# Optimization experiments

Hardware: AMD Instinct MI355X
Metric: run time of the kernel (lower is better)

Reference implementation:

```python
import jax, jax.numpy as jnp
import numpy as np

B, N, C = 1, 50000, 128
E, D = 800000, 2


def setup_inputs() -> dict:
    key = jax.random.key(0)
    k1, k2, k3 = jax.random.split(key, 3)
    x = jax.random.normal(k1, (B, N, C), dtype=jnp.float32)
    edge_weights = jax.random.normal(k2, (B, E, D), dtype=jnp.float32)
    directed_edges = jax.random.randint(k3, (B, E, 2), 0, N, dtype=jnp.int64)
    return {"x": x, "edge_weights": edge_weights, "directed_edges": directed_edges}


def reference(x, edge_weights, directed_edges):
    # x: [B, N, C] node features; edge_weights: [B, E, D]; directed_edges: [B, E, 2] = (target, source)
    b, n, c = x.shape
    _, e, d = edge_weights.shape
    target = directed_edges[..., 0]  # [B, E]
    source = directed_edges[..., 1]  # [B, E]
    bidx = jnp.arange(b)[:, None]  # [B, 1] broadcasts against [B, E]
    # gather node diffs per edge: [B, E, C]
    diff = x[bidx, source] - x[bidx, target]
    # weight by edge direction vector and flatten (C, D) -> C*D, matching torch reshape order
    message = jnp.einsum('bed,bec->becd', edge_weights, diff).reshape(b, e, c * d)
    # scatter-add into per-node gradient accumulator: [B, N, C*D]
    out = jnp.zeros((b, n, c * d), dtype=message.dtype)
    out = out.at[bidx, target].add(message)
    return out
```

## Files before the change

### kernel.cpp

```cpp
#include <hip/hip_runtime.h>


#define CAP 64
#define SCAN_TILE 512

__device__ __forceinline__ void gather_accum(const float* __restrict__ x,
                                             const int4* __restrict__ rec,
                                             int beg, int end, int lane,
                                             float& a0, float& a1, float& a2,
                                             float& a3, float& swx, float& swy) {
  int i = beg;
  for (; i + 4 <= end; i += 4) {
    const int4 r0 = rec[i];
    const int4 r1 = rec[i + 1];
    const int4 r2 = rec[i + 2];
    const int4 r3 = rec[i + 3];
    const float2 x0 = *reinterpret_cast<const float2*>(x + (size_t)r0.x * 128 + 2 * lane);
    const float2 x1 = *reinterpret_cast<const float2*>(x + (size_t)r1.x * 128 + 2 * lane);
    const float2 x2 = *reinterpret_cast<const float2*>(x + (size_t)r2.x * 128 + 2 * lane);
    const float2 x3 = *reinterpret_cast<const float2*>(x + (size_t)r3.x * 128 + 2 * lane);
    const float w0x = __int_as_float(r0.y), w0y = __int_as_float(r0.z);
    const float w1x = __int_as_float(r1.y), w1y = __int_as_float(r1.z);
    const float w2x = __int_as_float(r2.y), w2y = __int_as_float(r2.z);
    const float w3x = __int_as_float(r3.y), w3y = __int_as_float(r3.z);
    a0 += w0x * x0.x; a1 += w0y * x0.x; a2 += w0x * x0.y; a3 += w0y * x0.y;
    swx += w0x; swy += w0y;
    a0 += w1x * x1.x; a1 += w1y * x1.x; a2 += w1x * x1.y; a3 += w1y * x1.y;
    swx += w1x; swy += w1y;
    a0 += w2x * x2.x; a1 += w2y * x2.x; a2 += w2x * x2.y; a3 += w2y * x2.y;
    swx += w2x; swy += w2y;
    a0 += w3x * x3.x; a1 += w3y * x3.x; a2 += w3x * x3.y; a3 += w3y * x3.y;
    swx += w3x; swy += w3y;
  }
  for (; i < end; ++i) {
    const int4 r0 = rec[i];
    const float2 x0 = *reinterpret_cast<const float2*>(x + (size_t)r0.x * 128 + 2 * lane);
    const float w0x = __int_as_float(r0.y), w0y = __int_as_float(r0.z);
    a0 += w0x * x0.x; a1 += w0y * x0.x; a2 += w0x * x0.y; a3 += w0y * x0.y;
    swx += w0x; swy += w0y;
  }
}

__device__ __forceinline__ void gather_store(const float* __restrict__ x,
                                             float* __restrict__ out, int node,
                                             int lane, float a0, float a1, float a2,
                                             float a3, float swx, float swy) {
  const float2 xt = *reinterpret_cast<const float2*>(x + (size_t)node * 128 + 2 * lane);
  float4 o;
  o.x = a0 - swx * xt.x;
  o.y = a1 - swy * xt.x;
  o.z = a2 - swx * xt.y;
  o.w = a3 - swy * xt.y;
  *reinterpret_cast<float4*>(out + (size_t)node * 256 + 4 * lane) = o;
}

__global__ __launch_bounds__(256) void k_append(const int* __restrict__ edges,
                                                const float2* __restrict__ ew,
                                                int* __restrict__ counts,
                                                int4* __restrict__ rec, int E) {
  int e = blockIdx.x * blockDim.x + threadIdx.x;
  if (e >= E) return;
  const int2 ts = *reinterpret_cast<const int2*>(edges + 2ll * e);
  const float2 w = ew[e];
  const int pos = atomicAdd(&counts[ts.x], 1);
  if (pos < CAP) {
    int4 r;
    r.x = ts.y;
    r.y = __float_as_int(w.x);
    r.z = __float_as_int(w.y);
    r.w = 0;
    rec[(size_t)ts.x * CAP + pos] = r;
  }
}

__global__ __launch_bounds__(256) void k_gather_b(const float* __restrict__ x,
                                                  const int* __restrict__ counts,
                                                  const int4* __restrict__ rec,
                                                  float* __restrict__ out, int n) {
  const int lane = threadIdx.x & 63;
  const int node = (blockIdx.x * blockDim.x + threadIdx.x) >> 6;
  if (node >= n) return;
  const int deg = min(counts[node], CAP);
  const int beg = node * CAP;
  float a0 = 0.f, a1 = 0.f, a2 = 0.f, a3 = 0.f, swx = 0.f, swy = 0.f;
  gather_accum(x, rec, beg, beg + deg, lane, a0, a1, a2, a3, swx, swy);
  gather_store(x, out, node, lane, a0, a1, a2, a3, swx, swy);
}

__global__ __launch_bounds__(256) void k_hist(const int* __restrict__ edges,
                                              int* __restrict__ counts, int E) {
  int i = blockIdx.x * blockDim.x + threadIdx.x;
  int e = 2 * i;
  if (e + 1 < E) {
    int4 p = *reinterpret_cast<const int4*>(edges + 2ll * e);
    atomicAdd(&counts[p.x], 1);
    atomicAdd(&counts[p.z], 1);
  } else if (e < E) {
    atomicAdd(&counts[edges[2ll * e]], 1);
  }
}

__global__ __launch_bounds__(256) void k_part(const int* __restrict__ counts,
                                              int* __restrict__ partials, int n) {
  __shared__ int red[256];
  const int t = threadIdx.x;
  const int base = blockIdx.x * SCAN_TILE;
  int v = 0;
  int i0 = base + t, i1 = base + 256 + t;
  if (i0 < n) v += counts[i0];
  if (i1 < n) v += counts[i1];
  red[t] = v;
  __syncthreads();
  for (int s = 128; s > 0; s >>= 1) {
    if (t < s) red[t] += red[t + s];
    __syncthreads();
  }
  if (t == 0) partials[blockIdx.x] = red[0];
}

__global__ __launch_bounds__(1024) void k_scanp(int* __restrict__ partials, int P) {
  __shared__ int tile[1024];
  const int t = threadIdx.x;
  int v = (t < P) ? partials[t] : 0;
  tile[t] = v;
  __syncthreads();
  for (int off = 1; off < 1024; off <<= 1) {
    int u = (t >= off) ? tile[t - off] : 0;
    __syncthreads();
    tile[t] += u;
    __syncthreads();
  }
  if (t < P) partials[t] = tile[t] - v;
}

__global__ __launch_bounds__(256) void k_apply(const int* __restrict__ counts,
                                               const int* __restrict__ partials,
                                               int* __restrict__ offs,
                                               int* __restrict__ cursor, int n, int E) {
  __shared__ int tile[256];
  const int t = threadIdx.x;
  const int base = blockIdx.x * SCAN_TILE;
  const int ia = base + 2 * t, ib = ia + 1;
  int a = (ia < n) ? counts[ia] : 0;
  int b = (ib < n) ? counts[ib] : 0;
  int s = a + b;
  tile[t] = s;
  __syncthreads();
  for (int off = 1; off < 256; off <<= 1) {
    int u = (t >= off) ? tile[t - off] : 0;
    __syncthreads();
    tile[t] += u;
    __syncthreads();
  }
  const int excl = tile[t] - s;
  const int o = partials[blockIdx.x] + excl;
  if (ia < n) { offs[ia] = o; cursor[ia] = o; }
  if (ib < n) { offs[ib] = o + a; cursor[ib] = o + a; }
  if (blockIdx.x == 0 && t == 0) offs[n] = E;
}

__global__ __launch_bounds__(256) void k_scatter(const int* __restrict__ edges,
                                                 const float2* __restrict__ ew,
                                                 int* __restrict__ cursor,
                                                 int4* __restrict__ rec, int E) {
  int e = blockIdx.x * blockDim.x + threadIdx.x;
  if (e >= E) return;
  int2 ts = *reinterpret_cast<const int2*>(edges + 2ll * e);
  float2 w = ew[e];
  int pos = atomicAdd(&cursor[ts.x], 1);
  int4 r;
  r.x = ts.y;
  r.y = __float_as_int(w.x);
  r.z = __float_as_int(w.y);
  r.w = 0;
  rec[pos] = r;
}

__global__ __launch_bounds__(256) void k_gather_s(const float* __restrict__ x,
                                                  const int* __restrict__ offs,
                                                  const int4* __restrict__ rec,
                                                  float* __restrict__ out, int n) {
  const int lane = threadIdx.x & 63;
  const int node = (blockIdx.x * blockDim.x + threadIdx.x) >> 6;
  if (node >= n) return;
  float a0 = 0.f, a1 = 0.f, a2 = 0.f, a3 = 0.f, swx = 0.f, swy = 0.f;
  gather_accum(x, rec, offs[node], offs[node + 1], lane, a0, a1, a2, a3, swx, swy);
  gather_store(x, out, node, lane, a0, a1, a2, a3, swx, swy);
}

__global__ __launch_bounds__(256) void k_atomic(const float* __restrict__ x,
                                                const float* __restrict__ ew,
                                                const int* __restrict__ edges,
                                                float* __restrict__ out, int E) {
  const int lane = threadIdx.x & 63;
  const int wave = (blockIdx.x * blockDim.x + threadIdx.x) >> 6;
  const int nwaves = (gridDim.x * blockDim.x) >> 6;
  for (int e = wave; e < E; e += nwaves) {
    const int2 ts = *reinterpret_cast<const int2*>(edges + 2ll * e);
    const float2 w = *reinterpret_cast<const float2*>(ew + 2ll * e);
    const float2 vs = *reinterpret_cast<const float2*>(x + (size_t)ts.y * 128 + 2 * lane);
    const float2 vt = *reinterpret_cast<const float2*>(x + (size_t)ts.x * 128 + 2 * lane);
    const float d0 = vs.x - vt.x;
    const float d1 = vs.y - vt.y;
    float* o = out + (size_t)ts.x * 256 + 4 * lane;
    unsafeAtomicAdd(o + 0, w.x * d0);
    unsafeAtomicAdd(o + 1, w.y * d0);
    unsafeAtomicAdd(o + 2, w.x * d1);
    unsafeAtomicAdd(o + 3, w.y * d1);
  }
}

extern "C" void kernel_launch(void* const* d_in, const int* in_sizes, int n_in,
                              void* d_out, int out_size, void* d_ws, size_t ws_size,
                              hipStream_t stream) {
  const float* x = (const float*)d_in[0];
  const float* ewf = (const float*)d_in[1];
  const int* edges = (const int*)d_in[2];
  float* out = (float*)d_out;
  const float2* ew = (const float2*)ewf;

  const int E = in_sizes[1] / 2;
  const int N = in_sizes[0] / 128;

  size_t cnt_sec = ((size_t)N * 4 + 15) & ~(size_t)15;
  size_t need_bucket = cnt_sec + (size_t)N * CAP * 16;

  if (ws_size >= need_bucket) {
    char* wsb = (char*)d_ws;
    int* counts = (int*)wsb;
    int4* rec = (int4*)(wsb + cnt_sec);
    hipMemsetAsync(counts, 0, (size_t)N * 4, stream);
    k_append<<<(E + 255) / 256, 256, 0, stream>>>(edges, ew, counts, rec, E);
    k_gather_b<<<(N * 64 + 255) / 256, 256, 0, stream>>>(x, counts, rec, out, N);
    return;
  }

  const int P = (N + SCAN_TILE - 1) / SCAN_TILE;
  size_t int_sec = ((size_t)(3 * N + 1 + P) * 4 + 15) & ~(size_t)15;
  size_t need_sort = int_sec + (size_t)E * 16;

  if (ws_size >= need_sort) {
    char* wsb = (char*)d_ws;
    int* counts = (int*)wsb;
    int* offs = counts + N;
    int* cursor = offs + N + 1;
    int* partials = cursor + N;
    int4* rec = (int4*)(wsb + int_sec);
    hipMemsetAsync(counts, 0, (size_t)N * 4, stream);
    k_hist<<<((E + 1) / 2 + 255) / 256, 256, 0, stream>>>(edges, counts, E);
    k_part<<<P, 256, 0, stream>>>(counts, partials, N);
    k_scanp<<<1, 1024, 0, stream>>>(partials, P);
    k_apply<<<P, 256, 0, stream>>>(counts, partials, offs, cursor, N, E);
    k_scatter<<<(E + 255) / 256, 256, 0, stream>>>(edges, ew, cursor, rec, E);
    k_gather_s<<<(N * 64 + 255) / 256, 256, 0, stream>>>(x, offs, rec, out, N);
    return;
  }

  hipMemsetAsync(d_out, 0, (size_t)out_size * sizeof(float), stream);
  k_atomic<<<2048, 256, 0, stream>>>(x, ewf, edges, out, E);
}
```

Before: 115.3 us.

## Bucket edge indices instead of full records and split wave over two edges

The bucket path now stores only a 4-byte edge index per slot instead of a 16-byte record, so the append kernel writes far less and handles two edges per thread. The gather kernel loads one bucket entry per lane, looks up the source and weights, broadcasts them with shuffles, and has each half-wave process a different edge with float4 loads. A cross-half shuffle reduction then combines the partial sums before the store. In exchange, the gather does an extra indirect read of edges and weights, and the unrolled gather_accum used by the sort fallback path is simplified to a plain loop.

New measurement: 150.4 us. 30.5% more time.

```diff
diff --git a/kernel.cpp b/kernel.cpp
--- a/kernel.cpp
+++ b/kernel.cpp
@@ -3,88 +3,121 @@
 
 #define CAP 64
 #define SCAN_TILE 512
+
+__global__ __launch_bounds__(256) void k_append2(const int* __restrict__ edges,
+                                                 int* __restrict__ counts,
+                                                 int* __restrict__ idxb, int E) {
+  const int i = blockIdx.x * blockDim.x + threadIdx.x;
+  const int e = 2 * i;
+  if (e + 1 < E) {
+    const int4 p = *reinterpret_cast<const int4*>(edges + 2ll * e);
+    const int p0 = atomicAdd(&counts[p.x], 1);
+    if (p0 < CAP) idxb[p.x * CAP + p0] = e;
+    const int p1 = atomicAdd(&counts[p.z], 1);
+    if (p1 < CAP) idxb[p.z * CAP + p1] = e + 1;
+  } else if (e < E) {
+    const int t = edges[2ll * e];
+    const int p0 = atomicAdd(&counts[t], 1);
+    if (p0 < CAP) idxb[t * CAP + p0] = e;
+  }
+}
+
+#define ACC(xr, wx, wy)                                              \
+  a0 += (wx) * (xr).x; a1 += (wy) * (xr).x;                          \
+  a2 += (wx) * (xr).y; a3 += (wy) * (xr).y;                          \
+  a4 += (wx) * (xr).z; a5 += (wy) * (xr).z;                          \
+  a6 += (wx) * (xr).w; a7 += (wy) * (xr).w;                          \
+  swx += (wx); swy += (wy);
+
+__global__ __launch_bounds__(256) void k_gather2(const float* __restrict__ x,
+                                                 const int* __restrict__ counts,
+                                                 const int* __restrict__ idxb,
+                                                 const int* __restrict__ edges,
+                                                 const float2* __restrict__ ew,
+                                                 float* __restrict__ out, int n) {
+  const int lane = threadIdx.x & 63;
+  const int node = (blockIdx.x * blockDim.x + threadIdx.x) >> 6;
+  if (node >= n) return;
+  const int c = lane & 31;
+  const int half = lane >> 5;
+
+  const int deg = min(counts[node], CAP);
+
+  float a0 = 0.f, a1 = 0.f, a2 = 0.f, a3 = 0.f;
+  float a4 = 0.f, a5 = 0.f, a6 = 0.f, a7 = 0.f;
+  float swx = 0.f, swy = 0.f;
+
+  if (deg > 0) {
+    const int li = min(lane, deg - 1);
+    const int e = idxb[node * CAP + li];
+    const int srcl = edges[2 * e + 1];
+    const float2 wl = ew[e];
+
+    const int nfull = deg >> 1;
+    int i = 0;
+    for (; i + 2 <= nfull; i += 2) {
+      const int m0 = 2 * i + half;
+      const int m1 = m0 + 2;
+      const int s0 = __shfl(srcl, m0);
+      const float w0x = __shfl(wl.x, m0);
+      const float w0y = __shfl(wl.y, m0);
+      const int s1 = __shfl(srcl, m1);
+      const float w1x = __shfl(wl.x, m1);
+      const float w1y = __shfl(wl.y, m1);
+      const float4 x0 = *reinterpret_cast<const float4*>(x + (size_t)s0 * 128 + 4 * c);
+      const float4 x1 = *reinterpret_cast<const float4*>(x + (size_t)s1 * 128 + 4 * c);
+      ACC(x0, w0x, w0y)
+      ACC(x1, w1x, w1y)
+    }
+    if (i < nfull) {
+      const int m0 = 2 * i + half;
+      const int s0 = __shfl(srcl, m0);
+      const float w0x = __shfl(wl.x, m0);
+      const float w0y = __shfl(wl.y, m0);
+      const float4 x0 = *reinterpret_cast<const float4*>(x + (size_t)s0 * 128 + 4 * c);
+      ACC(x0, w0x, w0y)
+    }
+    if (deg & 1) {
+      const int m = deg - 1;
+      const int s0 = __shfl(srcl, m);
+      float w0x = __shfl(wl.x, m);
+      float w0y = __shfl(wl.y, m);
+      if (half) { w0x = 0.f; w0y = 0.f; }
+      const float4 x0 = *reinterpret_cast<const float4*>(x + (size_t)s0 * 128 + 4 * c);
+      ACC(x0, w0x, w0y)
+    }
+  }
+
+  a0 += __shfl_xor(a0, 32); a1 += __shfl_xor(a1, 32);
+  a2 += __shfl_xor(a2, 32); a3 += __shfl_xor(a3, 32);
+  a4 += __shfl_xor(a4, 32); a5 += __shfl_xor(a5, 32);
+  a6 += __shfl_xor(a6, 32); a7 += __shfl_xor(a7, 32);
+  swx += __shfl_xor(swx, 32); swy += __shfl_xor(swy, 32);
+
+  const float4 xt = *reinterpret_cast<const float4*>(x + (size_t)node * 128 + 4 * c);
+  float4 o;
+  if (half == 0) {
+    o.x = a0 - swx * xt.x; o.y = a1 - swy * xt.x;
+    o.z = a2 - swx * xt.y; o.w = a3 - swy * xt.y;
+  } else {
+    o.x = a4 - swx * xt.z; o.y = a5 - swy * xt.z;
+    o.z = a6 - swx * xt.w; o.w = a7 - swy * xt.w;
+  }
+  *reinterpret_cast<float4*>(out + (size_t)node * 256 + 8 * c + 4 * half) = o;
+}
 
 __device__ __forceinline__ void gather_accum(const float* __restrict__ x,
                                              const int4* __restrict__ rec,
                                              int beg, int end, int lane,
                                              float& a0, float& a1, float& a2,
                                              float& a3, float& swx, float& swy) {
-  int i = beg;
-  for (; i + 4 <= end; i += 4) {
-    const int4 r0 = rec[i];
-    const int4 r1 = rec[i + 1];
-    const int4 r2 = rec[i + 2];
-    const int4 r3 = rec[i + 3];
-    const float2 x0 = *reinterpret_cast<const float2*>(x + (size_t)r0.x * 128 + 2 * lane);
-    const float2 x1 = *reinterpret_cast<const float2*>(x + (size_t)r1.x * 128 + 2 * lane);
-    const float2 x2 = *reinterpret_cast<const float2*>(x + (size_t)r2.x * 128 + 2 * lane);
-    const float2 x3 = *reinterpret_cast<const float2*>(x + (size_t)r3.x * 128 + 2 * lane);
-    const float w0x = __int_as_float(r0.y), w0y = __int_as_float(r0.z);
-    const float w1x = __int_as_float(r1.y), w1y = __int_as_float(r1.z);
-    const float w2x = __int_as_float(r2.y), w2y = __int_as_float(r2.z);
-    const float w3x = __int_as_float(r3.y), w3y = __int_as_float(r3.z);
-    a0 += w0x * x0.x; a1 += w0y * x0.x; a2 += w0x * x0.y; a3 += w0y * x0.y;
-    swx += w0x; swy += w0y;
-    a0 += w1x * x1.x; a1 += w1y * x1.x; a2 += w1x * x1.y; a3 += w1y * x1.y;
-    swx += w1x; swy += w1y;
-    a0 += w2x * x2.x; a1 += w2y * x2.x; a2 += w2x * x2.y; a3 += w2y * x2.y;
-    swx += w2x; swy += w2y;
-    a0 += w3x * x3.x; a1 += w3y * x3.x; a2 += w3x * x3.y; a3 += w3y * x3.y;
-    swx += w3x; swy += w3y;
-  }
-  for (; i < end; ++i) {
+  for (int i = beg; i < end; ++i) {
     const int4 r0 = rec[i];
     const float2 x0 = *reinterpret_cast<const float2*>(x + (size_t)r0.x * 128 + 2 * lane);
     const float w0x = __int_as_float(r0.y), w0y = __int_as_float(r0.z);
     a0 += w0x * x0.x; a1 += w0y * x0.x; a2 += w0x * x0.y; a3 += w0y * x0.y;
     swx += w0x; swy += w0y;
   }
-}
-
-__device__ __forceinline__ void gather_store(const float* __restrict__ x,
-                                             float* __restrict__ out, int node,
-                                             int lane, float a0, float a1, float a2,
-                                             float a3, float swx, float swy) {
-  const float2 xt = *reinterpret_cast<const float2*>(x + (size_t)node * 128 + 2 * lane);
-  float4 o;
-  o.x = a0 - swx * xt.x;
-  o.y = a1 - swy * xt.x;
-  o.z = a2 - swx * xt.y;
-  o.w = a3 - swy * xt.y;
-  *reinterpret_cast<float4*>(out + (size_t)node * 256 + 4 * lane) = o;
-}
-
-__global__ __launch_bounds__(256) void k_append(const int* __restrict__ edges,
-                                                const float2* __restrict__ ew,
-                                                int* __restrict__ counts,
-                                                int4* __restrict__ rec, int E) {
-  int e = blockIdx.x * blockDim.x + threadIdx.x;
-  if (e >= E) return;
-  const int2 ts = *reinterpret_cast<const int2*>(edges + 2ll * e);
-  const float2 w = ew[e];
-  const int pos = atomicAdd(&counts[ts.x], 1);
-  if (pos < CAP) {
-    int4 r;
-    r.x = ts.y;
-    r.y = __float_as_int(w.x);
-    r.z = __float_as_int(w.y);
-    r.w = 0;
-    rec[(size_t)ts.x * CAP + pos] = r;
-  }
-}
-
-__global__ __launch_bounds__(256) void k_gather_b(const float* __restrict__ x,
-                                                  const int* __restrict__ counts,
-                                                  const int4* __restrict__ rec,
-                                                  float* __restrict__ out, int n) {
-  const int lane = threadIdx.x & 63;
-  const int node = (blockIdx.x * blockDim.x + threadIdx.x) >> 6;
-  if (node >= n) return;
-  const int deg = min(counts[node], CAP);
-  const int beg = node * CAP;
-  float a0 = 0.f, a1 = 0.f, a2 = 0.f, a3 = 0.f, swx = 0.f, swy = 0.f;
-  gather_accum(x, rec, beg, beg + deg, lane, a0, a1, a2, a3, swx, swy);
-  gather_store(x, out, node, lane, a0, a1, a2, a3, swx, swy);
 }
 
 __global__ __launch_bounds__(256) void k_hist(const int* __restrict__ edges,
@@ -185,7 +218,13 @@
   if (node >= n) return;
   float a0 = 0.f, a1 = 0.f, a2 = 0.f, a3 = 0.f, swx = 0.f, swy = 0.f;
   gather_accum(x, rec, offs[node], offs[node + 1], lane, a0, a1, a2, a3, swx, swy);
-  gather_store(x, out, node, lane, a0, a1, a2, a3, swx, swy);
+  const float2 xt = *reinterpret_cast<const float2*>(x + (size_t)node * 128 + 2 * lane);
+  float4 o;
+  o.x = a0 - swx * xt.x;
+  o.y = a1 - swy * xt.x;
+  o.z = a2 - swx * xt.y;
+  o.w = a3 - swy * xt.y;
+  *reinterpret_cast<float4*>(out + (size_t)node * 256 + 4 * lane) = o;
 }
 
 __global__ __launch_bounds__(256) void k_atomic(const float* __restrict__ x,
@@ -223,15 +262,15 @@
   const int N = in_sizes[0] / 128;
 
   size_t cnt_sec = ((size_t)N * 4 + 15) & ~(size_t)15;
-  size_t need_bucket = cnt_sec + (size_t)N * CAP * 16;
+  size_t need_bucket = cnt_sec + (size_t)N * CAP * 4;
 
   if (ws_size >= need_bucket) {
     char* wsb = (char*)d_ws;
     int* counts = (int*)wsb;
-    int4* rec = (int4*)(wsb + cnt_sec);
+    int* idxb = (int*)(wsb + cnt_sec);
     hipMemsetAsync(counts, 0, (size_t)N * 4, stream);
-    k_append<<<(E + 255) / 256, 256, 0, stream>>>(edges, ew, counts, rec, E);
-    k_gather_b<<<(N * 64 + 255) / 256, 256, 0, stream>>>(x, counts, rec, out, N);
+    k_append2<<<((E + 1) / 2 + 255) / 256, 256, 0, stream>>>(edges, counts, idxb, E);
+    k_gather2<<<(N * 64 + 255) / 256, 256, 0, stream>>>(x, counts, idxb, edges, ew, out, N);
     return;
   }
 
```

## Stage bucket records in LDS and split wave into half-waves over float4 rows

Applied to the files above, without the earlier changes.

The bucketed gather kernel now loads each node's edge records once per wave, one per lane, into shared memory. The weight sums come from a wave shuffle reduction instead of per-lane serial accumulation. Each half-wave handles alternating edges with float4 row loads and eight accumulators, and the two halves are combined with a shuffle at the end. This replaces redundant broadcast reads of the record list from global memory and halves the per-edge loop trip count, at the cost of a block-level barrier, more registers and extra shuffles. The sorted-path gather is inlined and loses its 4-way unrolling.

Result: no change. 113.4 us (-1.6%).

```diff
diff --git a/kernel.cpp b/kernel.cpp
--- a/kernel.cpp
+++ b/kernel.cpp
@@ -3,64 +3,14 @@
 
 #define CAP 64
 #define SCAN_TILE 512
-
-__device__ __forceinline__ void gather_accum(const float* __restrict__ x,
-                                             const int4* __restrict__ rec,
-                                             int beg, int end, int lane,
-                                             float& a0, float& a1, float& a2,
-                                             float& a3, float& swx, float& swy) {
-  int i = beg;
-  for (; i + 4 <= end; i += 4) {
-    const int4 r0 = rec[i];
-    const int4 r1 = rec[i + 1];
-    const int4 r2 = rec[i + 2];
-    const int4 r3 = rec[i + 3];
-    const float2 x0 = *reinterpret_cast<const float2*>(x + (size_t)r0.x * 128 + 2 * lane);
-    const float2 x1 = *reinterpret_cast<const float2*>(x + (size_t)r1.x * 128 + 2 * lane);
-    const float2 x2 = *reinterpret_cast<const float2*>(x + (size_t)r2.x * 128 + 2 * lane);
-    const float2 x3 = *reinterpret_cast<const float2*>(x + (size_t)r3.x * 128 + 2 * lane);
-    const float w0x = __int_as_float(r0.y), w0y = __int_as_float(r0.z);
-    const float w1x = __int_as_float(r1.y), w1y = __int_as_float(r1.z);
-    const float w2x = __int_as_float(r2.y), w2y = __int_as_float(r2.z);
-    const float w3x = __int_as_float(r3.y), w3y = __int_as_float(r3.z);
-    a0 += w0x * x0.x; a1 += w0y * x0.x; a2 += w0x * x0.y; a3 += w0y * x0.y;
-    swx += w0x; swy += w0y;
-    a0 += w1x * x1.x; a1 += w1y * x1.x; a2 += w1x * x1.y; a3 += w1y * x1.y;
-    swx += w1x; swy += w1y;
-    a0 += w2x * x2.x; a1 += w2y * x2.x; a2 += w2x * x2.y; a3 += w2y * x2.y;
-    swx += w2x; swy += w2y;
-    a0 += w3x * x3.x; a1 += w3y * x3.x; a2 += w3x * x3.y; a3 += w3y * x3.y;
-    swx += w3x; swy += w3y;
-  }
-  for (; i < end; ++i) {
-    const int4 r0 = rec[i];
-    const float2 x0 = *reinterpret_cast<const float2*>(x + (size_t)r0.x * 128 + 2 * lane);
-    const float w0x = __int_as_float(r0.y), w0y = __int_as_float(r0.z);
-    a0 += w0x * x0.x; a1 += w0y * x0.x; a2 += w0x * x0.y; a3 += w0y * x0.y;
-    swx += w0x; swy += w0y;
-  }
-}
-
-__device__ __forceinline__ void gather_store(const float* __restrict__ x,
-                                             float* __restrict__ out, int node,
-                                             int lane, float a0, float a1, float a2,
-                                             float a3, float swx, float swy) {
-  const float2 xt = *reinterpret_cast<const float2*>(x + (size_t)node * 128 + 2 * lane);
-  float4 o;
-  o.x = a0 - swx * xt.x;
-  o.y = a1 - swy * xt.x;
-  o.z = a2 - swx * xt.y;
-  o.w = a3 - swy * xt.y;
-  *reinterpret_cast<float4*>(out + (size_t)node * 256 + 4 * lane) = o;
-}
 
 __global__ __launch_bounds__(256) void k_append(const int* __restrict__ edges,
                                                 const float2* __restrict__ ew,
                                                 int* __restrict__ counts,
                                                 int4* __restrict__ rec, int E) {
-  int e = blockIdx.x * blockDim.x + threadIdx.x;
+  const int e = blockIdx.x * blockDim.x + threadIdx.x;
   if (e >= E) return;
-  const int2 ts = *reinterpret_cast<const int2*>(edges + 2ll * e);
+  const int2 ts = reinterpret_cast<const int2*>(edges)[e];
   const float2 w = ew[e];
   const int pos = atomicAdd(&counts[ts.x], 1);
   if (pos < CAP) {
@@ -73,18 +23,93 @@
   }
 }
 
-__global__ __launch_bounds__(256) void k_gather_b(const float* __restrict__ x,
-                                                  const int* __restrict__ counts,
-                                                  const int4* __restrict__ rec,
-                                                  float* __restrict__ out, int n) {
+#define ACC8(X, WX, WY)                                  \
+  a0 = fmaf((WX), (X).x, a0); a1 = fmaf((WY), (X).x, a1); \
+  a2 = fmaf((WX), (X).y, a2); a3 = fmaf((WY), (X).y, a3); \
+  a4 = fmaf((WX), (X).z, a4); a5 = fmaf((WY), (X).z, a5); \
+  a6 = fmaf((WX), (X).w, a6); a7 = fmaf((WY), (X).w, a7);
+
+__device__ __forceinline__ float4 ldrow(const float* __restrict__ x, int src, int c) {
+  return *reinterpret_cast<const float4*>(x + (size_t)src * 128 + 4 * c);
+}
+
+__global__ __launch_bounds__(256) void k_gather3(const float* __restrict__ x,
+                                                 const int* __restrict__ counts,
+                                                 const int4* __restrict__ rec,
+                                                 float* __restrict__ out, int n) {
+  __shared__ int4 smem[4][CAP];
   const int lane = threadIdx.x & 63;
+  const int wid = threadIdx.x >> 6;
   const int node = (blockIdx.x * blockDim.x + threadIdx.x) >> 6;
+  const int c = lane & 31;
+  const int half = lane >> 5;
+
+  int deg = 0;
+  int4 r = make_int4(0, 0, 0, 0);
+  if (node < n) {
+    deg = min(counts[node], CAP);
+    if (deg > 0) {
+      const int li = min(lane, deg - 1);
+      r = rec[(size_t)node * CAP + li];
+    }
+  }
+  int4 rs = r;
+  if (lane >= deg) { rs.y = 0; rs.z = 0; }
+  smem[wid][lane] = rs;
+  __syncthreads();
+
   if (node >= n) return;
-  const int deg = min(counts[node], CAP);
-  const int beg = node * CAP;
-  float a0 = 0.f, a1 = 0.f, a2 = 0.f, a3 = 0.f, swx = 0.f, swy = 0.f;
-  gather_accum(x, rec, beg, beg + deg, lane, a0, a1, a2, a3, swx, swy);
-  gather_store(x, out, node, lane, a0, a1, a2, a3, swx, swy);
+
+  float swx = (lane < deg) ? __int_as_float(r.y) : 0.f;
+  float swy = (lane < deg) ? __int_as_float(r.z) : 0.f;
+  for (int off = 1; off < 64; off <<= 1) {
+    swx += __shfl_xor(swx, off);
+    swy += __shfl_xor(swy, off);
+  }
+
+  float a0 = 0.f, a1 = 0.f, a2 = 0.f, a3 = 0.f;
+  float a4 = 0.f, a5 = 0.f, a6 = 0.f, a7 = 0.f;
+
+  const int4* sm = smem[wid];
+  const int npair = (deg + 1) >> 1;
+  int i = 0;
+  for (; i + 4 <= npair; i += 4) {
+    const int j0 = 2 * i + half;
+    const int4 m0 = sm[j0];
+    const int4 m1 = sm[j0 + 2];
+    const int4 m2 = sm[j0 + 4];
+    const int4 m3 = sm[j0 + 6];
+    const float4 X0 = ldrow(x, m0.x, c);
+    const float4 X1 = ldrow(x, m1.x, c);
+    const float4 X2 = ldrow(x, m2.x, c);
+    const float4 X3 = ldrow(x, m3.x, c);
+    ACC8(X0, __int_as_float(m0.y), __int_as_float(m0.z))
+    ACC8(X1, __int_as_float(m1.y), __int_as_float(m1.z))
+    ACC8(X2, __int_as_float(m2.y), __int_as_float(m2.z))
+    ACC8(X3, __int_as_float(m3.y), __int_as_float(m3.z))
+  }
+  for (; i < npair; ++i) {
+    const int j = 2 * i + half;
+    const int4 m = sm[j];
+    const float4 X = ldrow(x, m.x, c);
+    ACC8(X, __int_as_float(m.y), __int_as_float(m.z))
+  }
+
+  a0 += __shfl_xor(a0, 32); a1 += __shfl_xor(a1, 32);
+  a2 += __shfl_xor(a2, 32); a3 += __shfl_xor(a3, 32);
+  a4 += __shfl_xor(a4, 32); a5 += __shfl_xor(a5, 32);
+  a6 += __shfl_xor(a6, 32); a7 += __shfl_xor(a7, 32);
+
+  const float4 xt = ldrow(x, node, c);
+  float4 o;
+  if (half == 0) {
+    o.x = a0 - swx * xt.x; o.y = a1 - swy * xt.x;
+    o.z = a2 - swx * xt.y; o.w = a3 - swy * xt.y;
+  } else {
+    o.x = a4 - swx * xt.z; o.y = a5 - swy * xt.z;
+    o.z = a6 - swx * xt.w; o.w = a7 - swy * xt.w;
+  }
+  *reinterpret_cast<float4*>(out + (size_t)node * 256 + 8 * c + 4 * half) = o;
 }
 
 __global__ __launch_bounds__(256) void k_hist(const int* __restrict__ edges,
@@ -184,8 +209,20 @@
   const int node = (blockIdx.x * blockDim.x + threadIdx.x) >> 6;
   if (node >= n) return;
   float a0 = 0.f, a1 = 0.f, a2 = 0.f, a3 = 0.f, swx = 0.f, swy = 0.f;
-  gather_accum(x, rec, offs[node], offs[node + 1], lane, a0, a1, a2, a3, swx, swy);
-  gather_store(x, out, node, lane, a0, a1, a2, a3, swx, swy);
+  for (int i = offs[node]; i < offs[node + 1]; ++i) {
+    const int4 r0 = rec[i];
+    const float2 x0 = *reinterpret_cast<const float2*>(x + (size_t)r0.x * 128 + 2 * lane);
+    const float w0x = __int_as_float(r0.y), w0y = __int_as_float(r0.z);
+    a0 += w0x * x0.x; a1 += w0y * x0.x; a2 += w0x * x0.y; a3 += w0y * x0.y;
+    swx += w0x; swy += w0y;
+  }
+  const float2 xt = *reinterpret_cast<const float2*>(x + (size_t)node * 128 + 2 * lane);
+  float4 o;
+  o.x = a0 - swx * xt.x;
+  o.y = a1 - swy * xt.x;
+  o.z = a2 - swx * xt.y;
+  o.w = a3 - swy * xt.y;
+  *reinterpret_cast<float4*>(out + (size_t)node * 256 + 4 * lane) = o;
 }
 
 __global__ __launch_bounds__(256) void k_atomic(const float* __restrict__ x,
@@ -231,7 +268,7 @@
     int4* rec = (int4*)(wsb + cnt_sec);
     hipMemsetAsync(counts, 0, (size_t)N * 4, stream);
     k_append<<<(E + 255) / 256, 256, 0, stream>>>(edges, ew, counts, rec, E);
-    k_gather_b<<<(N * 64 + 255) / 256, 256, 0, stream>>>(x, counts, rec, out, N);
+    k_gather3<<<(N * 64 + 255) / 256, 256, 0, stream>>>(x, counts, rec, out, N);
     return;
   }
 
```
